# Performance work log

Measured on AMD Instinct MI355X. Metric: run time of the kernel, lower is better.

## Reference

```python
import jax, jax.numpy as jnp
import numpy as np

D_MODEL = 1024
N_HEADS = 16
D_HEAD = D_MODEL // N_HEADS


def setup_inputs() -> dict:
    key = jax.random.key(0)
    ks = jax.random.split(key, 11)
    B, S = 2, 2048
    scale = 1.0 / np.sqrt(D_MODEL)
    inp = {
        "query": jax.random.normal(ks[0], (B, S, D_MODEL), jnp.float32),
        "key": jax.random.normal(ks[1], (B, S, D_MODEL), jnp.float32),
        "value": jax.random.normal(ks[2], (B, S, D_MODEL), jnp.float32),
        "Wq": jax.random.normal(ks[3], (D_MODEL, D_MODEL), jnp.float32) * scale,
        "bq": jnp.zeros((D_MODEL,), jnp.float32),
        "Wk": jax.random.normal(ks[4], (D_MODEL, D_MODEL), jnp.float32) * scale,
        "bk": jnp.zeros((D_MODEL,), jnp.float32),
        "Wv": jax.random.normal(ks[5], (D_MODEL, D_MODEL), jnp.float32) * scale,
        "bv": jnp.zeros((D_MODEL,), jnp.float32),
        "Wo": jax.random.normal(ks[6], (D_MODEL, D_MODEL), jnp.float32) * scale,
        "bo": jnp.zeros((D_MODEL,), jnp.float32),
    }
    return inp


def _split_heads(x):
    B, S, _ = x.shape
    return x.reshape(B, S, N_HEADS, D_HEAD).transpose(0, 2, 1, 3)  # [B,H,S,Dh]


def reference(query, key, value, Wq, bq, Wk, bk, Wv, bv, Wo, bo):
    q = _split_heads(query @ Wq + bq)
    k = _split_heads(key @ Wk + bk)
    v = _split_heads(value @ Wv + bv)
    # scores [B,H,S,S] -- faithfully materialized as in the original
    scores = jnp.einsum("bhqd,bhkd->bhqk", q, k) / np.sqrt(D_HEAD)
    attn = jax.nn.softmax(scores, axis=-1)
    out = jnp.einsum("bhqk,bhkd->bhqd", attn, v)  # [B,H,S,Dh]
    B, H, S, Dh = out.shape
    out = out.transpose(0, 2, 1, 3).reshape(B, S, H * Dh)
    return out @ Wo + bo
```

## Files before the change

### kernel.cpp

```cpp
#include <hip/hip_runtime.h>
#include <hip/hip_bf16.h>

using bf16 = __hip_bfloat16;
typedef __bf16 bf16x8 __attribute__((ext_vector_type(8)));
typedef __bf16 bf16x2v __attribute__((ext_vector_type(2)));
typedef float f32x4 __attribute__((ext_vector_type(4)));

#define SEQ 2048
#define DM  1024
#define QSCALE 0.18033688011112042f

__device__ __forceinline__ f32x4 mfma16(bf16x8 a, bf16x8 b, f32x4 c) {
  return __builtin_amdgcn_mfma_f32_16x16x32_bf16(a, b, c, 0, 0, 0);
}
__device__ __forceinline__ void gload16(const void* g, void* l) {
  __builtin_amdgcn_global_load_lds(
      (const __attribute__((address_space(1))) unsigned int*)g,
      (__attribute__((address_space(3))) unsigned int*)l, 16, 0, 0);
}
__device__ __forceinline__ unsigned short bfbits(float x) {
  bf16 h = __float2bfloat16(x);
  return *reinterpret_cast<unsigned short*>(&h);
}
__device__ __forceinline__ unsigned pk2(float a, float b) {
#if __has_builtin(__builtin_amdgcn_cvt_pk_bf16_f32)
  bf16x2v r = __builtin_amdgcn_cvt_pk_bf16_f32(a, b);
  return *reinterpret_cast<unsigned*>(&r);
#else
  return (unsigned)bfbits(a) | ((unsigned)bfbits(b) << 16);
#endif
}
__device__ __forceinline__ float fexp2(float x) {
#if __has_builtin(__builtin_amdgcn_exp2f)
  return __builtin_amdgcn_exp2f(x);
#else
  return exp2f(x);
#endif
}

__global__ __launch_bounds__(256) void cast_x(const float* __restrict__ q,
                                              const float* __restrict__ k,
                                              const float* __restrict__ v,
                                              bf16* __restrict__ Lx) {
  const float* src = blockIdx.y == 0 ? q : (blockIdx.y == 1 ? k : v);
  bf16* dst = Lx + (size_t)blockIdx.y * (4096ull * 1024) + (size_t)blockIdx.x * 16384;
#pragma unroll
  for (int i = 0; i < 8; ++i) {
    int u = threadIdx.x + i * 256;
    int k32 = u >> 6, l = u & 63;
    const float* p = src + (size_t)(blockIdx.x * 16 + (l & 15)) * 1024 + k32 * 32 + (l >> 4) * 8;
    float4 a = *(const float4*)p;
    float4 b = *(const float4*)(p + 4);
    alignas(16) unsigned o[4] = {pk2(a.x, a.y), pk2(a.z, a.w), pk2(b.x, b.y), pk2(b.z, b.w)};
    *(uint4*)(dst + (size_t)u * 8) = *(const uint4*)o;
  }
}

__global__ __launch_bounds__(256) void cast_w(const float* __restrict__ Wq,
                                              const float* __restrict__ Wk,
                                              const float* __restrict__ Wv,
                                              const float* __restrict__ Wo,
                                              bf16* __restrict__ Lw,
                                              bf16* __restrict__ Lwo) {
  const int widx = blockIdx.z;
  const float* W = widx == 0 ? Wq : (widx == 1 ? Wk : (widx == 2 ? Wv : Wo));
  bf16* dst = widx < 3 ? (Lw + (size_t)widx * 1048576) : Lwo;
  __shared__ float tf[64][68];
  const int t = threadIdx.x, bx = blockIdx.x, by = blockIdx.y;
#pragma unroll
  for (int i = 0; i < 4; ++i) {
    int u = t + i * 256, r = u >> 4, c4 = u & 15;
    *(float4*)&tf[r][c4 * 4] = *(const float4*)(W + (size_t)(by * 64 + r) * 1024 + bx * 64 + c4 * 4);
  }
  __syncthreads();
#pragma unroll
  for (int i = 0; i < 2; ++i) {
    int u = t + i * 256;
    int sub = u >> 6, l = u & 63;
    int n16l = sub >> 1, k32l = sub & 1;
    int nn = n16l * 16 + (l & 15);
    int kk = k32l * 32 + (l >> 4) * 8;
    alignas(16) unsigned o[4];
#pragma unroll
    for (int p = 0; p < 4; ++p) o[p] = pk2(tf[kk + 2 * p][nn], tf[kk + 2 * p + 1][nn]);
    size_t off = ((((size_t)(bx * 4 + n16l)) * 32 + (by * 2 + k32l)) * 64 + l) * 8;
    *(uint4*)(dst + off) = *(const uint4*)o;
  }
}

__global__ __launch_bounds__(256) void qkv_gemm(const bf16* __restrict__ Lw,
                                                const bf16* __restrict__ Lx,
                                                const float* __restrict__ bq,
                                                const float* __restrict__ bk,
                                                const float* __restrict__ bv,
                                                bf16* __restrict__ Lq,
                                                bf16* __restrict__ Lk,
                                                bf16* __restrict__ Lv) {
  __shared__ alignas(16) bf16 Wl[8192];
  __shared__ alignas(16) bf16 Xl[8192];
  const int t = threadIdx.x, lane = t & 63, w = t >> 6;
  const int m16 = lane & 15, g4 = lane >> 4;
  const int third = blockIdx.y >> 3, mtl = blockIdx.y & 7, nt = blockIdx.x;
  const int wm = w >> 1, wn = w & 1;
  const bf16* Wb = Lw + (size_t)third * 1048576;
  const bf16* Xb = Lx + (size_t)third * (4096ull * 1024);
  f32x4 acc[4][4] = {};

  for (int slab = 0; slab < 16; ++slab) {
#pragma unroll
    for (int ii = 0; ii < 4; ++ii) {
      int s = w * 4 + ii;
      const bf16* gp = Wb + ((((size_t)(mtl * 8 + (s >> 1))) * 32 + slab * 2 + (s & 1)) * 64 + lane) * 8;
      gload16(gp, (void*)&Wl[s * 512]);
    }
#pragma unroll
    for (int ii = 0; ii < 4; ++ii) {
      int s = w * 4 + ii;
      const bf16* gp = Xb + ((((size_t)(nt * 8 + (s >> 1))) * 32 + slab * 2 + (s & 1)) * 64 + lane) * 8;
      gload16(gp, (void*)&Xl[s * 512]);
    }
    __syncthreads();
#pragma unroll
    for (int c = 0; c < 2; ++c) {
      bf16x8 wf[4], xf[4];
#pragma unroll
      for (int i = 0; i < 4; ++i) wf[i] = *(const bf16x8*)&Wl[((wm * 4 + i) * 2 + c) * 512 + lane * 8];
#pragma unroll
      for (int j = 0; j < 4; ++j) xf[j] = *(const bf16x8*)&Xl[((wn * 4 + j) * 2 + c) * 512 + lane * 8];
      if (third < 2) {
#pragma unroll
        for (int i = 0; i < 4; ++i)
#pragma unroll
          for (int j = 0; j < 4; ++j) acc[i][j] = mfma16(wf[i], xf[j], acc[i][j]);
      } else {
#pragma unroll
        for (int i = 0; i < 4; ++i)
#pragma unroll
          for (int j = 0; j < 4; ++j) acc[i][j] = mfma16(xf[i], wf[j], acc[i][j]);
      }
    }
    __syncthreads();
  }

  if (third < 2) {
    bf16* dst = third == 0 ? Lq : Lk;
    const float* bias = third == 0 ? bq : bk;
    const float sc = third == 0 ? QSCALE : 1.0f;
#pragma unroll
    for (int i = 0; i < 4; ++i) {
      int doutb = mtl * 128 + wm * 64 + i * 16 + g4 * 4;
      float4 b4 = *(const float4*)(bias + doutb);
      int hh = doutb >> 6, d32 = (doutb & 63) >> 5;
      int lhi = (doutb & 31) >> 3, half = g4 & 1;
#pragma unroll
      for (int j = 0; j < 4; ++j) {
        int seq = nt * 128 + wn * 64 + j * 16 + m16;
        int bb = seq >> 11, s16w = (seq & 2047) >> 4;
        size_t off = ((((size_t)(bb * 128 + s16w)) * 16 + hh) * 2 + d32) * 512 + (m16 + 16 * lhi) * 8 + half * 4;
        uint2 pv;
        pv.x = pk2((acc[i][j][0] + b4.x) * sc, (acc[i][j][1] + b4.y) * sc);
        pv.y = pk2((acc[i][j][2] + b4.z) * sc, (acc[i][j][3] + b4.w) * sc);
        *(uint2*)(dst + off) = pv;
      }
    }
  } else {
#pragma unroll
    for (int j = 0; j < 4; ++j) {
      int dout = mtl * 128 + wm * 64 + j * 16 + m16;
      float bvv = bv[dout];
      int hh = dout >> 6, dt = (dout & 63) >> 4;
#pragma unroll
      for (int i = 0; i < 4; ++i) {
        int seqb = nt * 128 + wn * 64 + i * 16 + g4 * 4;
        int bb = seqb >> 11, kt = (seqb & 2047) >> 6, ks32 = (seqb & 63) >> 5;
        int lhi = (seqb & 31) >> 3, half = g4 & 1;
        size_t off = (((((size_t)(bb * 32 + kt)) * 16 + hh) * 4 + dt) * 2 + ks32) * 512 + (m16 + 16 * lhi) * 8 + half * 4;
        uint2 pv;
        pv.x = pk2(acc[i][j][0] + bvv, acc[i][j][1] + bvv);
        pv.y = pk2(acc[i][j][2] + bvv, acc[i][j][3] + bvv);
        *(uint2*)(Lv + off) = pv;
      }
    }
  }
}

__global__ __launch_bounds__(512, 4) void flash(const bf16* __restrict__ Lq,
                                                const bf16* __restrict__ Lk,
                                                const bf16* __restrict__ Lv,
                                                bf16* __restrict__ Lab) {
  __shared__ alignas(16) unsigned char smem[51200];
  bf16* const Kb = (bf16*)smem;
  bf16* const Vb = (bf16*)(smem + 16384);
  bf16* const Pt = (bf16*)(smem + 32768);

  const int t = threadIdx.x, lane = t & 63, w = t >> 6;
  const int m16 = lane & 15, g4 = lane >> 4;
  const int wg = w & 3, g = w >> 2;
  const int bid = blockIdx.x;
  const int logical = ((bid & 7) << 6) | (bid >> 3);
  const int qt = logical & 15, h = (logical >> 4) & 15, b = logical >> 8;

  bf16* const Ptw = Pt + w * (32 * 36);

  bf16x8 qf[2][2];
#pragma unroll
  for (int q2 = 0; q2 < 2; ++q2)
#pragma unroll
    for (int ks = 0; ks < 2; ++ks)
      qf[q2][ks] = *(const bf16x8*)(Lq +
          ((((size_t)(b * 128 + qt * 8 + wg * 2 + q2)) * 16 + h) * 2 + ks) * 512 + lane * 8);

  const int s16l = wg >> 1, d32 = wg & 1;
  {
    const bf16* gk = Lk + ((((size_t)(b * 128 + g * 64 + s16l)) * 16 + h) * 2 + d32) * 512 + lane * 8;
    gload16(gk, (void*)(Kb + (g * 2 + 0) * 2048 + wg * 512));
    const bf16* gv = Lv + (((((size_t)(b * 32 + g * 16)) * 16 + h) * 4 + wg) * 2 + 0) * 512 + lane * 8;
    gload16(gv, (void*)(Vb + (g * 2 + 0) * 2048 + wg * 512));
  }

  float lrow[2] = {0.f, 0.f};
  f32x4 oacc[4][2] = {};
  __syncthreads();

  for (int kt = 0; kt < 32; ++kt) {
    const int cur = kt & 1;
    const bf16* const Kl = Kb + (g * 2 + cur) * 2048;
    const bf16* const Vl = Vb + (g * 2 + cur) * 2048;
    if (kt < 31) {
      const int nkt = kt + 1, nb = cur ^ 1;
      const bf16* gk = Lk + ((((size_t)(b * 128 + g * 64 + nkt * 2 + s16l)) * 16 + h) * 2 + d32) * 512 + lane * 8;
      gload16(gk, (void*)(Kb + (g * 2 + nb) * 2048 + wg * 512));
      const bf16* gv = Lv + (((((size_t)(b * 32 + g * 16 + (nkt >> 1))) * 16 + h) * 4 + wg) * 2 + (nkt & 1)) * 512 + lane * 8;
      gload16(gv, (void*)(Vb + (g * 2 + nb) * 2048 + wg * 512));
    }

    f32x4 s[2][2] = {};
#pragma unroll
    for (int ks = 0; ks < 2; ++ks) {
      bf16x8 aK[2];
#pragma unroll
      for (int mt = 0; mt < 2; ++mt) aK[mt] = *(const bf16x8*)&Kl[(mt * 2 + ks) * 512 + lane * 8];
#pragma unroll
      for (int mt = 0; mt < 2; ++mt)
#pragma unroll
        for (int q2 = 0; q2 < 2; ++q2) s[mt][q2] = mfma16(aK[mt], qf[q2][ks], s[mt][q2]);
    }

#pragma unroll
    for (int q2 = 0; q2 < 2; ++q2)
#pragma unroll
      for (int mt = 0; mt < 2; ++mt) {
        float e0 = fexp2(s[mt][q2][0]);
        float e1 = fexp2(s[mt][q2][1]);
        float e2 = fexp2(s[mt][q2][2]);
        float e3 = fexp2(s[mt][q2][3]);
        lrow[q2] += (e0 + e1) + (e2 + e3);
        uint2 pv;
        pv.x = pk2(e0, e1);
        pv.y = pk2(e2, e3);
        *(uint2*)&Ptw[(q2 * 16 + m16) * 36 + mt * 16 + g4 * 4] = pv;
      }

    {
      bf16x8 aV[4], bP[2];
#pragma unroll
      for (int dt = 0; dt < 4; ++dt) aV[dt] = *(const bf16x8*)&Vl[dt * 512 + lane * 8];
#pragma unroll
      for (int q2 = 0; q2 < 2; ++q2) {
        alignas(16) unsigned tmp[4];
        *(uint2*)&tmp[0] = *(const uint2*)&Ptw[(q2 * 16 + m16) * 36 + g4 * 8];
        *(uint2*)&tmp[2] = *(const uint2*)&Ptw[(q2 * 16 + m16) * 36 + g4 * 8 + 4];
        bP[q2] = *(const bf16x8*)tmp;
      }
#pragma unroll
      for (int dt = 0; dt < 4; ++dt)
#pragma unroll
        for (int q2 = 0; q2 < 2; ++q2) oacc[dt][q2] = mfma16(aV[dt], bP[q2], oacc[dt][q2]);
    }
    __syncthreads();
  }

#pragma unroll
  for (int q2 = 0; q2 < 2; ++q2) {
    lrow[q2] += __shfl_xor(lrow[q2], 16);
    lrow[q2] += __shfl_xor(lrow[q2], 32);
  }

  float* const Os = (float*)smem;
  float* const Ls = (float*)(smem + 32768);
  if (w >= 4) {
#pragma unroll
    for (int dt = 0; dt < 4; ++dt)
#pragma unroll
      for (int q2 = 0; q2 < 2; ++q2)
        *(f32x4*)&Os[(((wg * 4 + dt) * 2 + q2) * 64 + lane) * 4] = oacc[dt][q2];
    if (g4 == 0) {
      Ls[(wg * 2 + 0) * 16 + m16] = lrow[0];
      Ls[(wg * 2 + 1) * 16 + m16] = lrow[1];
    }
  }
  __syncthreads();
  if (w < 4) {
#pragma unroll
    for (int q2 = 0; q2 < 2; ++q2) {
      float inv = 1.f / (lrow[q2] + Ls[(wg * 2 + q2) * 16 + m16]);
      int q = b * 2048 + qt * 128 + w * 32 + q2 * 16 + m16;
      int s16g = q >> 4;
#pragma unroll
      for (int dt = 0; dt < 4; ++dt) {
        f32x4 p = *(const f32x4*)&Os[(((wg * 4 + dt) * 2 + q2) * 64 + lane) * 4];
        int dbase = h * 64 + dt * 16 + g4 * 4;
        int k32 = dbase >> 5, lhi = (dbase & 31) >> 3, half = g4 & 1;
        size_t off = ((size_t)s16g * 32 + k32) * 512 + (m16 + 16 * lhi) * 8 + half * 4;
        uint2 pv;
        pv.x = pk2((oacc[dt][q2][0] + p[0]) * inv, (oacc[dt][q2][1] + p[1]) * inv);
        pv.y = pk2((oacc[dt][q2][2] + p[2]) * inv, (oacc[dt][q2][3] + p[3]) * inv);
        *(uint2*)(Lab + off) = pv;
      }
    }
  }
}

__global__ __launch_bounds__(256) void out_gemm(const bf16* __restrict__ Lab,
                                                const bf16* __restrict__ Lwo,
                                                const float* __restrict__ bo,
                                                float* __restrict__ out) {
  __shared__ alignas(16) bf16 Al[8192];
  __shared__ alignas(16) bf16 Bl[4096];
  const int t = threadIdx.x, lane = t & 63, w = t >> 6;
  const int m16 = lane & 15, g4 = lane >> 4;
  const int nt = blockIdx.x, mt = blockIdx.y;
  const int wm = w >> 1, wn = w & 1;
  f32x4 acc[4][2] = {};

  for (int slab = 0; slab < 16; ++slab) {
#pragma unroll
    for (int ii = 0; ii < 4; ++ii) {
      int s = w * 4 + ii;
      const bf16* gp = Lab + (((size_t)(mt * 8 + (s >> 1))) * 32 + slab * 2 + (s & 1)) * 512 + lane * 8;
      gload16(gp, (void*)&Al[s * 512]);
    }
#pragma unroll
    for (int ii = 0; ii < 2; ++ii) {
      int s = w * 2 + ii;
      const bf16* gp = Lwo + (((size_t)(nt * 4 + (s >> 1))) * 32 + slab * 2 + (s & 1)) * 512 + lane * 8;
      gload16(gp, (void*)&Bl[s * 512]);
    }
    __syncthreads();
#pragma unroll
    for (int c = 0; c < 2; ++c) {
      bf16x8 aA[4], bW[2];
#pragma unroll
      for (int i = 0; i < 4; ++i) aA[i] = *(const bf16x8*)&Al[((wm * 4 + i) * 2 + c) * 512 + lane * 8];
#pragma unroll
      for (int j = 0; j < 2; ++j) bW[j] = *(const bf16x8*)&Bl[((wn * 2 + j) * 2 + c) * 512 + lane * 8];
#pragma unroll
      for (int i = 0; i < 4; ++i)
#pragma unroll
        for (int j = 0; j < 2; ++j) acc[i][j] = mfma16(aA[i], bW[j], acc[i][j]);
    }
    __syncthreads();
  }
#pragma unroll
  for (int j = 0; j < 2; ++j) {
    int n = nt * 64 + wn * 32 + j * 16 + m16;
    float bb = bo[n];
#pragma unroll
    for (int i = 0; i < 4; ++i) {
      int seqb = mt * 128 + wm * 64 + i * 16 + g4 * 4;
#pragma unroll
      for (int r = 0; r < 4; ++r) out[(size_t)(seqb + r) * 1024 + n] = acc[i][j][r] + bb;
    }
  }
}

extern "C" void kernel_launch(void* const* d_in, const int* in_sizes, int n_in,
                              void* d_out, int out_size, void* d_ws, size_t ws_size,
                              hipStream_t stream) {
  const float* query = (const float*)d_in[0];
  const float* key   = (const float*)d_in[1];
  const float* value = (const float*)d_in[2];
  const float* Wq = (const float*)d_in[3];
  const float* bq = (const float*)d_in[4];
  const float* Wk = (const float*)d_in[5];
  const float* bk = (const float*)d_in[6];
  const float* Wv = (const float*)d_in[7];
  const float* bv = (const float*)d_in[8];
  const float* Wo = (const float*)d_in[9];
  const float* bo = (const float*)d_in[10];
  float* out = (float*)d_out;

  bf16* Lw  = (bf16*)d_ws;
  bf16* Lwo = Lw + 3ull * 1048576;
  bf16* Lx  = Lwo + 1048576;
  bf16* Lq  = Lx + 3ull * 4194304;
  bf16* Lk  = Lq + 4194304;
  bf16* Lv  = Lk + 4194304;
  bf16* Lab = Lv + 4194304;

  cast_x<<<dim3(256, 3), 256, 0, stream>>>(query, key, value, Lx);
  cast_w<<<dim3(16, 16, 4), 256, 0, stream>>>(Wq, Wk, Wv, Wo, Lw, Lwo);
  qkv_gemm<<<dim3(32, 24), 256, 0, stream>>>(Lw, Lx, bq, bk, bv, Lq, Lk, Lv);
  flash<<<512, 512, 0, stream>>>(Lq, Lk, Lv, Lab);
  out_gemm<<<dim3(16, 32), 256, 0, stream>>>(Lab, Lwo, bo, out);
}
```

Measured before the change: 215.8 us.

## Switch flash attention to 32x32 MFMA with register-resident P and merge cast kernels

Rewrites the flash kernel to use 32x32x16 bf16 MFMA tiles, which keeps the P matrix in registers by exchanging halves with v_permlane32_swap instead of staging it through LDS. Each iteration now loads two 64-key chunks (bigger double buffers, 64KB LDS) and s_setprio is raised around the MFMA blocks. The two cast kernels are merged into one launch to save a kernel launch. The trade-off is higher register and LDS use per block, which may lower occupancy, and the non-max-subtracted softmax is kept unchanged.

Result: no change. 215.2 us (-0.3%).

```diff
diff --git a/kernel.cpp b/kernel.cpp
--- a/kernel.cpp
+++ b/kernel.cpp
@@ -5,6 +5,7 @@
 typedef __bf16 bf16x8 __attribute__((ext_vector_type(8)));
 typedef __bf16 bf16x2v __attribute__((ext_vector_type(2)));
 typedef float f32x4 __attribute__((ext_vector_type(4)));
+typedef float f32x16 __attribute__((ext_vector_type(16)));
 
 #define SEQ 2048
 #define DM  1024
@@ -12,6 +13,9 @@
 
 __device__ __forceinline__ f32x4 mfma16(bf16x8 a, bf16x8 b, f32x4 c) {
   return __builtin_amdgcn_mfma_f32_16x16x32_bf16(a, b, c, 0, 0, 0);
+}
+__device__ __forceinline__ f32x16 mfma32(bf16x8 a, bf16x8 b, f32x16 c) {
+  return __builtin_amdgcn_mfma_f32_32x32x16_bf16(a, b, c, 0, 0, 0);
 }
 __device__ __forceinline__ void gload16(const void* g, void* l) {
   __builtin_amdgcn_global_load_lds(
@@ -37,36 +41,40 @@
   return exp2f(x);
 #endif
 }
-
-__global__ __launch_bounds__(256) void cast_x(const float* __restrict__ q,
-                                              const float* __restrict__ k,
-                                              const float* __restrict__ v,
-                                              bf16* __restrict__ Lx) {
-  const float* src = blockIdx.y == 0 ? q : (blockIdx.y == 1 ? k : v);
-  bf16* dst = Lx + (size_t)blockIdx.y * (4096ull * 1024) + (size_t)blockIdx.x * 16384;
-#pragma unroll
-  for (int i = 0; i < 8; ++i) {
-    int u = threadIdx.x + i * 256;
-    int k32 = u >> 6, l = u & 63;
-    const float* p = src + (size_t)(blockIdx.x * 16 + (l & 15)) * 1024 + k32 * 32 + (l >> 4) * 8;
-    float4 a = *(const float4*)p;
-    float4 b = *(const float4*)(p + 4);
-    alignas(16) unsigned o[4] = {pk2(a.x, a.y), pk2(a.z, a.w), pk2(b.x, b.y), pk2(b.z, b.w)};
-    *(uint4*)(dst + (size_t)u * 8) = *(const uint4*)o;
-  }
-}
-
-__global__ __launch_bounds__(256) void cast_w(const float* __restrict__ Wq,
-                                              const float* __restrict__ Wk,
-                                              const float* __restrict__ Wv,
-                                              const float* __restrict__ Wo,
-                                              bf16* __restrict__ Lw,
-                                              bf16* __restrict__ Lwo) {
-  const int widx = blockIdx.z;
+__device__ __forceinline__ void plswap(unsigned& a, unsigned& b) {
+  asm("v_permlane32_swap_b32 %0, %1" : "+v"(a), "+v"(b));
+}
+
+__global__ __launch_bounds__(256) void cast_all(const float* __restrict__ q,
+                                                const float* __restrict__ k,
+                                                const float* __restrict__ v,
+                                                const float* __restrict__ Wq,
+                                                const float* __restrict__ Wk,
+                                                const float* __restrict__ Wv,
+                                                const float* __restrict__ Wo,
+                                                bf16* __restrict__ Lx,
+                                                bf16* __restrict__ Lw,
+                                                bf16* __restrict__ Lwo) {
+  __shared__ float tf[64][68];
+  if (blockIdx.y < 3) {
+    const float* src = blockIdx.y == 0 ? q : (blockIdx.y == 1 ? k : v);
+    bf16* dst = Lx + (size_t)blockIdx.y * (4096ull * 1024) + (size_t)blockIdx.x * 16384;
+#pragma unroll
+    for (int i = 0; i < 8; ++i) {
+      int u = threadIdx.x + i * 256;
+      int k32 = u >> 6, l = u & 63;
+      const float* p = src + (size_t)(blockIdx.x * 16 + (l & 15)) * 1024 + k32 * 32 + (l >> 4) * 8;
+      float4 a = *(const float4*)p;
+      float4 b = *(const float4*)(p + 4);
+      alignas(16) unsigned o[4] = {pk2(a.x, a.y), pk2(a.z, a.w), pk2(b.x, b.y), pk2(b.z, b.w)};
+      *(uint4*)(dst + (size_t)u * 8) = *(const uint4*)o;
+    }
+    return;
+  }
+  const int widx = blockIdx.y - 3;
   const float* W = widx == 0 ? Wq : (widx == 1 ? Wk : (widx == 2 ? Wv : Wo));
   bf16* dst = widx < 3 ? (Lw + (size_t)widx * 1048576) : Lwo;
-  __shared__ float tf[64][68];
-  const int t = threadIdx.x, bx = blockIdx.x, by = blockIdx.y;
+  const int t = threadIdx.x, bx = blockIdx.x & 15, by = blockIdx.x >> 4;
 #pragma unroll
   for (int i = 0; i < 4; ++i) {
     int u = t + i * 256, r = u >> 4, c4 = u & 15;
@@ -188,134 +196,134 @@
                                                 const bf16* __restrict__ Lk,
                                                 const bf16* __restrict__ Lv,
                                                 bf16* __restrict__ Lab) {
-  __shared__ alignas(16) unsigned char smem[51200];
+  __shared__ alignas(16) unsigned char smem[65536];
   bf16* const Kb = (bf16*)smem;
-  bf16* const Vb = (bf16*)(smem + 16384);
-  bf16* const Pt = (bf16*)(smem + 32768);
+  bf16* const Vb = (bf16*)(smem + 32768);
 
   const int t = threadIdx.x, lane = t & 63, w = t >> 6;
-  const int m16 = lane & 15, g4 = lane >> 4;
-  const int wg = w & 3, g = w >> 2;
+  const int l31 = lane & 31, m16 = lane & 15, hi = lane >> 5, b4 = (lane >> 4) & 1;
+  const int qw = w >> 1, g = w & 1, wg = w >> 1;
   const int bid = blockIdx.x;
   const int logical = ((bid & 7) << 6) | (bid >> 3);
   const int qt = logical & 15, h = (logical >> 4) & 15, b = logical >> 8;
 
-  bf16* const Ptw = Pt + w * (32 * 36);
-
-  bf16x8 qf[2][2];
-#pragma unroll
-  for (int q2 = 0; q2 < 2; ++q2)
-#pragma unroll
-    for (int ks = 0; ks < 2; ++ks)
-      qf[q2][ks] = *(const bf16x8*)(Lq +
-          ((((size_t)(b * 128 + qt * 8 + wg * 2 + q2)) * 16 + h) * 2 + ks) * 512 + lane * 8);
-
-  const int s16l = wg >> 1, d32 = wg & 1;
+  bf16x8 qf[4];
   {
-    const bf16* gk = Lk + ((((size_t)(b * 128 + g * 64 + s16l)) * 16 + h) * 2 + d32) * 512 + lane * 8;
-    gload16(gk, (void*)(Kb + (g * 2 + 0) * 2048 + wg * 512));
-    const bf16* gv = Lv + (((((size_t)(b * 32 + g * 16)) * 16 + h) * 4 + wg) * 2 + 0) * 512 + lane * 8;
-    gload16(gv, (void*)(Vb + (g * 2 + 0) * 2048 + wg * 512));
-  }
-
-  float lrow[2] = {0.f, 0.f};
-  f32x4 oacc[4][2] = {};
+    const int sQ = b * 128 + qt * 8 + qw * 2 + b4;
+#pragma unroll
+    for (int ks = 0; ks < 4; ++ks) {
+      const int d32 = ks >> 1, g4q = (ks & 1) * 2 + hi;
+      qf[ks] = *(const bf16x8*)(Lq + (((size_t)sQ * 16 + h) * 2 + d32) * 512 + (m16 + 16 * g4q) * 8);
+    }
+  }
+
+  const int ss = wg >> 1, sd = wg & 1;
+#pragma unroll
+  for (int u = 0; u < 2; ++u) {
+    const bf16* gk = Lk + ((((size_t)(b * 128 + g * 64 + u * 2 + ss)) * 16 + h) * 2 + sd) * 512 + lane * 8;
+    gload16(gk, (void*)(Kb + (g * 2 + 0) * 4096 + u * 2048 + wg * 512));
+    const bf16* gv = Lv + (((((size_t)(b * 32 + g * 16)) * 16 + h) * 4 + wg) * 2 + u) * 512 + lane * 8;
+    gload16(gv, (void*)(Vb + (g * 2 + 0) * 4096 + u * 2048 + wg * 512));
+  }
+
+  float lrow = 0.f;
+  f32x16 oacc[2] = {};
   __syncthreads();
 
-  for (int kt = 0; kt < 32; ++kt) {
-    const int cur = kt & 1;
-    const bf16* const Kl = Kb + (g * 2 + cur) * 2048;
-    const bf16* const Vl = Vb + (g * 2 + cur) * 2048;
-    if (kt < 31) {
-      const int nkt = kt + 1, nb = cur ^ 1;
-      const bf16* gk = Lk + ((((size_t)(b * 128 + g * 64 + nkt * 2 + s16l)) * 16 + h) * 2 + d32) * 512 + lane * 8;
-      gload16(gk, (void*)(Kb + (g * 2 + nb) * 2048 + wg * 512));
-      const bf16* gv = Lv + (((((size_t)(b * 32 + g * 16 + (nkt >> 1))) * 16 + h) * 4 + wg) * 2 + (nkt & 1)) * 512 + lane * 8;
-      gload16(gv, (void*)(Vb + (g * 2 + nb) * 2048 + wg * 512));
-    }
-
-    f32x4 s[2][2] = {};
-#pragma unroll
-    for (int ks = 0; ks < 2; ++ks) {
-      bf16x8 aK[2];
-#pragma unroll
-      for (int mt = 0; mt < 2; ++mt) aK[mt] = *(const bf16x8*)&Kl[(mt * 2 + ks) * 512 + lane * 8];
-#pragma unroll
-      for (int mt = 0; mt < 2; ++mt)
-#pragma unroll
-        for (int q2 = 0; q2 < 2; ++q2) s[mt][q2] = mfma16(aK[mt], qf[q2][ks], s[mt][q2]);
-    }
-
-#pragma unroll
-    for (int q2 = 0; q2 < 2; ++q2)
-#pragma unroll
-      for (int mt = 0; mt < 2; ++mt) {
-        float e0 = fexp2(s[mt][q2][0]);
-        float e1 = fexp2(s[mt][q2][1]);
-        float e2 = fexp2(s[mt][q2][2]);
-        float e3 = fexp2(s[mt][q2][3]);
-        lrow[q2] += (e0 + e1) + (e2 + e3);
-        uint2 pv;
-        pv.x = pk2(e0, e1);
-        pv.y = pk2(e2, e3);
-        *(uint2*)&Ptw[(q2 * 16 + m16) * 36 + mt * 16 + g4 * 4] = pv;
-      }
-
-    {
-      bf16x8 aV[4], bP[2];
-#pragma unroll
-      for (int dt = 0; dt < 4; ++dt) aV[dt] = *(const bf16x8*)&Vl[dt * 512 + lane * 8];
-#pragma unroll
-      for (int q2 = 0; q2 < 2; ++q2) {
-        alignas(16) unsigned tmp[4];
-        *(uint2*)&tmp[0] = *(const uint2*)&Ptw[(q2 * 16 + m16) * 36 + g4 * 8];
-        *(uint2*)&tmp[2] = *(const uint2*)&Ptw[(q2 * 16 + m16) * 36 + g4 * 8 + 4];
-        bP[q2] = *(const bf16x8*)tmp;
-      }
-#pragma unroll
-      for (int dt = 0; dt < 4; ++dt)
-#pragma unroll
-        for (int q2 = 0; q2 < 2; ++q2) oacc[dt][q2] = mfma16(aV[dt], bP[q2], oacc[dt][q2]);
+  for (int it = 0; it < 16; ++it) {
+    const int cur = it & 1;
+    const bf16* const Klb = Kb + (g * 2 + cur) * 4096;
+    const bf16* const Vlb = Vb + (g * 2 + cur) * 4096;
+    if (it < 15) {
+      const int nb = cur ^ 1;
+#pragma unroll
+      for (int u = 0; u < 2; ++u) {
+        const int kc = (it + 1) * 2 + u;
+        const bf16* gk = Lk + ((((size_t)(b * 128 + g * 64 + kc * 2 + ss)) * 16 + h) * 2 + sd) * 512 + lane * 8;
+        gload16(gk, (void*)(Kb + (g * 2 + nb) * 4096 + u * 2048 + wg * 512));
+        const bf16* gv = Lv + (((((size_t)(b * 32 + g * 16 + (kc >> 1))) * 16 + h) * 4 + wg) * 2 + (kc & 1)) * 512 + lane * 8;
+        gload16(gv, (void*)(Vb + (g * 2 + nb) * 4096 + u * 2048 + wg * 512));
+      }
+    }
+
+#pragma unroll
+    for (int u = 0; u < 2; ++u) {
+      const bf16* const Kl = Klb + u * 2048;
+      const bf16* const Vl = Vlb + u * 2048;
+
+      f32x16 s = {};
+      __builtin_amdgcn_s_setprio(1);
+#pragma unroll
+      for (int ks = 0; ks < 4; ++ks) {
+        const int d32 = ks >> 1, g4k = (ks & 1) * 2 + hi;
+        bf16x8 kf = *(const bf16x8*)&Kl[((b4 * 2 + d32) * 64 + m16 + 16 * g4k) * 8];
+        s = mfma32(kf, qf[ks], s);
+      }
+      __builtin_amdgcn_s_setprio(0);
+
+      float e[16];
+#pragma unroll
+      for (int r = 0; r < 16; ++r) e[r] = fexp2(s[r]);
+      {
+        float a0 = e[0] + e[1], a1 = e[2] + e[3], a2 = e[4] + e[5], a3 = e[6] + e[7];
+        float a4 = e[8] + e[9], a5 = e[10] + e[11], a6 = e[12] + e[13], a7 = e[14] + e[15];
+        lrow += ((a0 + a1) + (a2 + a3)) + ((a4 + a5) + (a6 + a7));
+      }
+      bf16x8 bP[2];
+#pragma unroll
+      for (int c = 0; c < 2; ++c) {
+        unsigned P0 = pk2(e[8 * c + 0], e[8 * c + 1]);
+        unsigned P1 = pk2(e[8 * c + 2], e[8 * c + 3]);
+        unsigned P2 = pk2(e[8 * c + 4], e[8 * c + 5]);
+        unsigned P3 = pk2(e[8 * c + 6], e[8 * c + 7]);
+        plswap(P0, P2);
+        plswap(P1, P3);
+        alignas(16) unsigned pw[4] = {P0, P1, P2, P3};
+        bP[c] = *(const bf16x8*)pw;
+      }
+
+      __builtin_amdgcn_s_setprio(1);
+#pragma unroll
+      for (int dtile = 0; dtile < 2; ++dtile) {
+        const int dt = dtile * 2 + b4;
+#pragma unroll
+        for (int c = 0; c < 2; ++c) {
+          bf16x8 av = *(const bf16x8*)&Vl[(dt * 64 + m16 + 16 * (2 * c + hi)) * 8];
+          oacc[dtile] = mfma32(av, bP[c], oacc[dtile]);
+        }
+      }
+      __builtin_amdgcn_s_setprio(0);
     }
     __syncthreads();
   }
 
-#pragma unroll
-  for (int q2 = 0; q2 < 2; ++q2) {
-    lrow[q2] += __shfl_xor(lrow[q2], 16);
-    lrow[q2] += __shfl_xor(lrow[q2], 32);
-  }
+  lrow += __shfl_xor(lrow, 32);
 
   float* const Os = (float*)smem;
   float* const Ls = (float*)(smem + 32768);
-  if (w >= 4) {
-#pragma unroll
-    for (int dt = 0; dt < 4; ++dt)
-#pragma unroll
-      for (int q2 = 0; q2 < 2; ++q2)
-        *(f32x4*)&Os[(((wg * 4 + dt) * 2 + q2) * 64 + lane) * 4] = oacc[dt][q2];
-    if (g4 == 0) {
-      Ls[(wg * 2 + 0) * 16 + m16] = lrow[0];
-      Ls[(wg * 2 + 1) * 16 + m16] = lrow[1];
-    }
+  if (g == 1) {
+#pragma unroll
+    for (int dtile = 0; dtile < 2; ++dtile)
+#pragma unroll
+      for (int r = 0; r < 16; ++r)
+        Os[((qw * 2 + dtile) * 16 + r) * 64 + lane] = oacc[dtile][r];
+    if (hi == 0) Ls[qw * 32 + l31] = lrow;
   }
   __syncthreads();
-  if (w < 4) {
-#pragma unroll
-    for (int q2 = 0; q2 < 2; ++q2) {
-      float inv = 1.f / (lrow[q2] + Ls[(wg * 2 + q2) * 16 + m16]);
-      int q = b * 2048 + qt * 128 + w * 32 + q2 * 16 + m16;
-      int s16g = q >> 4;
-#pragma unroll
-      for (int dt = 0; dt < 4; ++dt) {
-        f32x4 p = *(const f32x4*)&Os[(((wg * 4 + dt) * 2 + q2) * 64 + lane) * 4];
-        int dbase = h * 64 + dt * 16 + g4 * 4;
-        int k32 = dbase >> 5, lhi = (dbase & 31) >> 3, half = g4 & 1;
-        size_t off = ((size_t)s16g * 32 + k32) * 512 + (m16 + 16 * lhi) * 8 + half * 4;
-        uint2 pv;
-        pv.x = pk2((oacc[dt][q2][0] + p[0]) * inv, (oacc[dt][q2][1] + p[1]) * inv);
-        pv.y = pk2((oacc[dt][q2][2] + p[2]) * inv, (oacc[dt][q2][3] + p[3]) * inv);
-        *(uint2*)(Lab + off) = pv;
+  if (g == 0) {
+    const float inv = 1.f / (lrow + Ls[qw * 32 + l31]);
+    const int sQ = b * 128 + qt * 8 + qw * 2 + b4;
+#pragma unroll
+    for (int dtile = 0; dtile < 2; ++dtile) {
+      const int k32 = h * 2 + dtile;
+#pragma unroll
+      for (int j = 0; j < 8; ++j) {
+        const int r = 2 * j;
+        float o0 = oacc[dtile][r] + Os[((qw * 2 + dtile) * 16 + r) * 64 + lane];
+        float o1 = oacc[dtile][r + 1] + Os[((qw * 2 + dtile) * 16 + r + 1) * 64 + lane];
+        unsigned pv = pk2(o0 * inv, o1 * inv);
+        size_t off = ((size_t)sQ * 32 + k32) * 512 + (m16 + 16 * (r >> 2)) * 8 + 4 * hi + (r & 3);
+        *(unsigned*)(Lab + off) = pv;
       }
     }
   }
@@ -398,8 +406,7 @@
   bf16* Lv  = Lk + 4194304;
   bf16* Lab = Lv + 4194304;
 
-  cast_x<<<dim3(256, 3), 256, 0, stream>>>(query, key, value, Lx);
-  cast_w<<<dim3(16, 16, 4), 256, 0, stream>>>(Wq, Wk, Wv, Wo, Lw, Lwo);
+  cast_all<<<dim3(256, 7), 256, 0, stream>>>(query, key, value, Wq, Wk, Wv, Wo, Lx, Lw, Lwo);
   qkv_gemm<<<dim3(32, 24), 256, 0, stream>>>(Lw, Lx, bq, bk, bv, Lq, Lk, Lv);
   flash<<<512, 512, 0, stream>>>(Lq, Lk, Lv, Lab);
   out_gemm<<<dim3(16, 32), 256, 0, stream>>>(Lab, Lwo, bo, out);
```
